# Performance work log

Measured on AMD Instinct MI355X. Metric: run time of the kernel, lower is better.

## Reference

```python
import jax, jax.numpy as jnp
import numpy as np

B, L, H, NH = 8, 384, 512, 8
DH = H // NH
MAX_SEQ_LEN = 384


def setup_inputs() -> dict:
    key = jax.random.key(0)
    ks = jax.random.split(key, 16)
    s = 0.02
    seq_len = jnp.concatenate([
        jnp.array([L], dtype=jnp.int32),
        jax.random.randint(ks[3], (B - 1,), L // 2, L + 1, dtype=jnp.int32),
    ])
    return {
        "key": jax.random.normal(ks[0], (B, L, H), jnp.float32),
        "query": jax.random.normal(ks[1], (B, L, H), jnp.float32),
        "value": jax.random.normal(ks[2], (B, L, H), jnp.float32),
        "seq_len": seq_len,
        "pe": jax.random.normal(ks[4], (2 * MAX_SEQ_LEN + 1, H), jnp.float32) * s,
        "Wk": jax.random.normal(ks[5], (H, H), jnp.float32) * s,
        "bk": jnp.zeros((H,), jnp.float32),
        "Wq": jax.random.normal(ks[6], (H, H), jnp.float32) * s,
        "bq": jnp.zeros((H,), jnp.float32),
        "Wv": jax.random.normal(ks[7], (H, H), jnp.float32) * s,
        "bv": jnp.zeros((H,), jnp.float32),
        "Wr": jax.random.normal(ks[8], (H, H), jnp.float32) * s,
        "br": jnp.zeros((H,), jnp.float32),
        "u_bias": jax.random.normal(ks[9], (NH, DH), jnp.float32) * s,
        "v_bias": jax.random.normal(ks[10], (NH, DH), jnp.float32) * s,
        "Wff": jax.random.normal(ks[11], (H, H), jnp.float32) * s,
        "bff": jnp.zeros((H,), jnp.float32),
    }


def reference(key, query, value, seq_len, pe, Wk, bk, Wq, bq, Wv, bv, Wr, br, u_bias, v_bias, Wff, bff):
    # relative distances: rel[i, j] = j - i, in [-(L-1), L-1]
    rel = jnp.arange(L)[None, :] - jnp.arange(L)[:, None]          # [L, L]
    rpe = pe[rel + MAX_SEQ_LEN]                                    # [L, L, H]

    k = (key @ Wk.T + bk).reshape(B, L, NH, DH)
    q = (query @ Wq.T + bq).reshape(B, L, NH, DH)
    v = (value @ Wv.T + bv).reshape(B, L, NH, DH)
    rpe = (rpe @ Wr.T + br).reshape(L, L, NH, DH)

    # Transformer-XL score terms
    A = jnp.einsum('bihd,bjhd->bhij', q, k)                        # content-content
    Bt = jnp.einsum('bihd,ijhd->bhij', q, rpe)                     # content-position
    C = jnp.einsum('hd,bjhd->bhj', u_bias, k)[:, :, None, :]       # global content bias
    Dt = jnp.einsum('hd,ijhd->hij', v_bias, rpe)[None]             # global position bias

    scores = (A + Bt + C + Dt) / jnp.sqrt(jnp.float32(DH))
    key_mask = jnp.arange(L)[None, :] < seq_len[:, None]           # [B, L]
    scores = jnp.where(key_mask[:, None, None, :], scores, -1e15)
    attn = jax.nn.softmax(scores, axis=-1)                         # [B, NH, L, L]

    out = jnp.einsum('bhij,bjhd->bihd', attn, v).reshape(B, L, H)
    return out @ Wff.T + bff
```

## Files before the change

### kernel.cpp

```cpp
#include <hip/hip_runtime.h>
#include <hip/hip_bf16.h>

#define B_  8
#define L_  384
#define H_  512
#define NH_ 8
#define DH_ 64
#define RRM 768

typedef short bf16x8 __attribute__((ext_vector_type(8)));
typedef float f32x4  __attribute__((ext_vector_type(4)));
#define MFMA_BF16 __builtin_amdgcn_mfma_f32_16x16x32_bf16

static __device__ __forceinline__ unsigned short f2bf(float f) {
    unsigned u = __builtin_bit_cast(unsigned, f);
    u += 0x7fffu + ((u >> 16) & 1u);
    return (unsigned short)(u >> 16);
}
static __device__ __forceinline__ float bf2f(unsigned short s) {
    unsigned u = ((unsigned)s) << 16;
    return __builtin_bit_cast(float, u);
}

typedef unsigned int u32;
static __device__ __forceinline__ void glds16(const void* g, void* l) {
    __builtin_amdgcn_global_load_lds(
        (const __attribute__((address_space(1))) u32*)g,
        (__attribute__((address_space(3))) u32*)l, 16, 0, 0);
}

struct CvtArgs {
    const float* src[9];
    unsigned short* dst[9];
    int nchunks[9];
};
__global__ __launch_bounds__(256) void cvt_kernel(CvtArgs a) {
    int chunk = blockIdx.x;
    int r = 0;
    while (r < 8 && chunk >= a.nchunks[r]) { chunk -= a.nchunks[r]; r++; }
    const float4 v = ((const float4*)a.src[r])[chunk * 256 + threadIdx.x];
    ushort4 o;
    o.x = f2bf(v.x); o.y = f2bf(v.y); o.z = f2bf(v.z); o.w = f2bf(v.w);
    ((ushort4*)a.dst[r])[chunk * 256 + threadIdx.x] = o;
}

template <bool IS_FF>
__global__ __launch_bounds__(256) void gemm_nt(
    const unsigned short* __restrict__ A0, const unsigned short* __restrict__ A1,
    const unsigned short* __restrict__ A2, const unsigned short* __restrict__ A3,
    const unsigned short* __restrict__ A4,
    const unsigned short* __restrict__ W0, const unsigned short* __restrict__ W1,
    const unsigned short* __restrict__ W2, const unsigned short* __restrict__ W3,
    const unsigned short* __restrict__ W4,
    const float* __restrict__ b0, const float* __restrict__ b1,
    const float* __restrict__ b2, const float* __restrict__ b3,
    const float* __restrict__ b4,
    const float* __restrict__ ub, const float* __restrict__ vbias,
    unsigned short* __restrict__ qu, unsigned short* __restrict__ qv,
    unsigned short* __restrict__ kb, unsigned short* __restrict__ vT,
    unsigned short* __restrict__ rp, float* __restrict__ ff) {

    const int z = IS_FF ? 4 : blockIdx.z;
    if (!IS_FF && z == 3 && blockIdx.y >= 12) return;
    const unsigned short* A = z == 0 ? A0 : z == 1 ? A1 : z == 2 ? A2 : z == 3 ? A3 : A4;
    const unsigned short* W = z == 0 ? W0 : z == 1 ? W1 : z == 2 ? W2 : z == 3 ? W3 : W4;
    const float* bias       = z == 0 ? b0 : z == 1 ? b1 : z == 2 ? b2 : z == 3 ? b3 : b4;

    __shared__ unsigned short AsF[2 * 64 * 64];
    __shared__ unsigned short BsF[2 * 64 * 64];

    const int tid = threadIdx.x;
    const int w = tid >> 6, lane = tid & 63;
    const int quad = lane >> 4, lm = lane & 15;
    const int wr = (w & 1) * 32, wc = (w >> 1) * 32;

    const int sr = lane >> 3, sj = lane & 7;
    const unsigned short* ga = A + (size_t)(blockIdx.y * 64 + w * 16 + sr) * 512 + (sj ^ sr) * 8;
    const unsigned short* gb = W + (size_t)(blockIdx.x * 64 + w * 16 + sr) * 512 + (sj ^ sr) * 8;

    auto stage = [&](int kc, int buf) {
        #pragma unroll
        for (int t = 0; t < 2; ++t) {
            int off = buf * 4096 + (w * 16 + t * 8) * 64;
            off = __builtin_amdgcn_readfirstlane(off);
            glds16(ga + kc * 64 + t * 8 * 512, &AsF[off]);
            glds16(gb + kc * 64 + t * 8 * 512, &BsF[off]);
        }
    };

    f32x4 acc[2][2] = {};
    stage(0, 0);
    for (int kc = 0; kc < 8; ++kc) {
        __syncthreads();
        const int buf = kc & 1;
        if (kc < 7) stage(kc + 1, buf ^ 1);
        const int base = buf * 4096;
        #pragma unroll
        for (int ks = 0; ks < 2; ++ks) {
            const int s = (((ks * 4 + quad) ^ (lm & 7))) * 8;
            bf16x8 a0 = *(const bf16x8*)&AsF[base + (wr + lm) * 64 + s];
            bf16x8 a1 = *(const bf16x8*)&AsF[base + (wr + 16 + lm) * 64 + s];
            bf16x8 w0 = *(const bf16x8*)&BsF[base + (wc + lm) * 64 + s];
            bf16x8 w1 = *(const bf16x8*)&BsF[base + (wc + 16 + lm) * 64 + s];
            acc[0][0] = MFMA_BF16(a0, w0, acc[0][0], 0, 0, 0);
            acc[0][1] = MFMA_BF16(a0, w1, acc[0][1], 0, 0, 0);
            acc[1][0] = MFMA_BF16(a1, w0, acc[1][0], 0, 0, 0);
            acc[1][1] = MFMA_BF16(a1, w1, acc[1][1], 0, 0, 0);
        }
    }

    #pragma unroll
    for (int si = 0; si < 2; ++si) {
        #pragma unroll
        for (int sj2 = 0; sj2 < 2; ++sj2) {
            #pragma unroll
            for (int reg = 0; reg < 4; ++reg) {
                const int r = blockIdx.y * 64 + wr + si * 16 + quad * 4 + reg;
                const int c = blockIdx.x * 64 + wc + sj2 * 16 + lm;
                const float val = acc[si][sj2][reg] + bias[c];
                if (IS_FF) {
                    ff[r * 512 + c] = val;
                } else if (z == 0) {
                    const int bb = r / L_, ii = r - bb * L_;
                    const int h = c >> 6, d = c & 63;
                    const int idx = ((bb * NH_ + h) * L_ + ii) * DH_ + d;
                    qu[idx] = f2bf((val + ub[c]) * 0.125f);
                    qv[idx] = f2bf((val + vbias[c]) * 0.125f);
                } else if (z == 1) {
                    const int bb = r / L_, ii = r - bb * L_;
                    const int h = c >> 6, d = c & 63;
                    kb[((bb * NH_ + h) * L_ + ii) * DH_ + d] = f2bf(val);
                } else if (z == 2) {
                    const int bb = r / L_, ii = r - bb * L_;
                    const int h = c >> 6, d = c & 63;
                    vT[((bb * NH_ + h) * DH_ + d) * L_ + ii] = f2bf(val);
                } else {
                    rp[r * 512 + c] = f2bf(val);
                }
            }
        }
    }
}

#define BTSTR 424
__global__ __launch_bounds__(256) void attn_fused(
    const unsigned short* __restrict__ qu, const unsigned short* __restrict__ qv,
    const unsigned short* __restrict__ kbf, const unsigned short* __restrict__ vT,
    const unsigned short* __restrict__ rp, const int* __restrict__ seq_len,
    unsigned short* __restrict__ Obf) {
    __shared__ __align__(16) unsigned short BtP[32 * BTSTR];
    __shared__ float mx_red[32][2];
    __shared__ float sm_red[32][2];
    const int lane = threadIdx.x & 63, wv = threadIdx.x >> 6;
    const int quad = lane >> 4, lm = lane & 15;
    const int bh = blockIdx.y, b = bh >> 3, h = bh & 7;
    const int i0 = blockIdx.x * 32;
    const int sl = seq_len[b];
    const int msub = wv & 1, nh = wv >> 1;
    const int m_lo = 353 - i0;
    const int i_fr = i0 + msub * 16 + lm;

    {
        const unsigned short* qvr = qv + (size_t)(bh * L_ + i_fr) * DH_;
        const bf16x8 av0 = *(const bf16x8*)(qvr + quad * 8);
        const bf16x8 av1 = *(const bf16x8*)(qvr + 32 + quad * 8);
        #pragma unroll
        for (int ns = 0; ns < 13; ++ns) {
            const int ntl = nh * 208 + ns * 16;
            if (ntl <= sl + 30) {
                const int n = ntl + lm;
                const unsigned short* rrow = rp + (size_t)(m_lo + n) * 512 + h * 64;
                f32x4 bacc = {};
                bacc = MFMA_BF16(av0, *(const bf16x8*)(rrow + quad * 8), bacc, 0, 0, 0);
                bacc = MFMA_BF16(av1, *(const bf16x8*)(rrow + 32 + quad * 8), bacc, 0, 0, 0);
                #pragma unroll
                for (int reg = 0; reg < 4; ++reg) {
                    const int il = msub * 16 + quad * 4 + reg;
                    BtP[il * BTSTR + n] = f2bf(bacc[reg]);
                }
            }
        }
    }
    const unsigned short* qur = qu + (size_t)(bh * L_ + i_fr) * DH_;
    const bf16x8 au0 = *(const bf16x8*)(qur + quad * 8);
    const bf16x8 au1 = *(const bf16x8*)(qur + 32 + quad * 8);
    __syncthreads();

    f32x4 sc[12];
    #pragma unroll
    for (int ns = 0; ns < 12; ++ns) {
        const int jt = nh * 192 + ns * 16;
        if (jt < sl) {
            const unsigned short* krow = kbf + (size_t)(bh * L_ + jt + lm) * DH_;
            f32x4 a = {};
            a = MFMA_BF16(au0, *(const bf16x8*)(krow + quad * 8), a, 0, 0, 0);
            a = MFMA_BF16(au1, *(const bf16x8*)(krow + 32 + quad * 8), a, 0, 0, 0);
            sc[ns] = a;
        } else {
            sc[ns] = f32x4{-1e30f, -1e30f, -1e30f, -1e30f};
        }
    }
    const int jbase = nh * 192 + lm;
    #pragma unroll
    for (int ns = 0; ns < 12; ++ns) {
        const int j = jbase + ns * 16;
        #pragma unroll
        for (int reg = 0; reg < 4; ++reg) {
            const int il = msub * 16 + quad * 4 + reg;
            float val = -1e30f;
            if (j < sl) val = sc[ns][reg] + bf2f(BtP[il * BTSTR + (j - il + 31)]);
            sc[ns][reg] = val;
        }
    }

    const int il0 = msub * 16 + quad * 4;
    float mx4[4], sm4[4], inv4[4];
    #pragma unroll
    for (int reg = 0; reg < 4; ++reg) {
        float m = sc[0][reg];
        #pragma unroll
        for (int ns = 1; ns < 12; ++ns) m = fmaxf(m, sc[ns][reg]);
        #pragma unroll
        for (int o = 1; o < 16; o <<= 1) m = fmaxf(m, __shfl_xor(m, o));
        mx4[reg] = m;
    }
    if (lm == 0) {
        #pragma unroll
        for (int reg = 0; reg < 4; ++reg) mx_red[il0 + reg][nh] = mx4[reg];
    }
    __syncthreads();
    #pragma unroll
    for (int reg = 0; reg < 4; ++reg)
        mx4[reg] = fmaxf(mx_red[il0 + reg][0], mx_red[il0 + reg][1]);
    #pragma unroll
    for (int reg = 0; reg < 4; ++reg) sm4[reg] = 0.f;
    #pragma unroll
    for (int ns = 0; ns < 12; ++ns) {
        #pragma unroll
        for (int reg = 0; reg < 4; ++reg) {
            const float e = __expf(sc[ns][reg] - mx4[reg]);
            sc[ns][reg] = e;
            sm4[reg] += e;
        }
    }
    #pragma unroll
    for (int reg = 0; reg < 4; ++reg) {
        float s = sm4[reg];
        #pragma unroll
        for (int o = 1; o < 16; o <<= 1) s += __shfl_xor(s, o);
        sm4[reg] = s;
    }
    if (lm == 0) {
        #pragma unroll
        for (int reg = 0; reg < 4; ++reg) sm_red[il0 + reg][nh] = sm4[reg];
    }
    __syncthreads();
    #pragma unroll
    for (int reg = 0; reg < 4; ++reg)
        inv4[reg] = 1.f / (sm_red[il0 + reg][0] + sm_red[il0 + reg][1]);

    #pragma unroll
    for (int ns = 0; ns < 12; ++ns) {
        const int j = jbase + ns * 16;
        #pragma unroll
        for (int reg = 0; reg < 4; ++reg)
            BtP[(il0 + reg) * BTSTR + j] = f2bf(sc[ns][reg] * inv4[reg]);
    }
    __syncthreads();

    {
        const int pr = msub * 16 + lm;
        const int nkc = (sl + 31) >> 5;
        f32x4 oacc[2] = {};
        for (int kc = 0; kc < nkc; ++kc) {
            const bf16x8 af = *(const bf16x8*)&BtP[pr * BTSTR + kc * 32 + quad * 8];
            #pragma unroll
            for (int t = 0; t < 2; ++t) {
                const int n = nh * 32 + t * 16 + lm;
                const unsigned short* vrow = vT + (size_t)(bh * DH_ + n) * L_ + kc * 32 + quad * 8;
                oacc[t] = MFMA_BF16(af, *(const bf16x8*)(vrow), oacc[t], 0, 0, 0);
            }
        }
        #pragma unroll
        for (int t = 0; t < 2; ++t) {
            #pragma unroll
            for (int reg = 0; reg < 4; ++reg) {
                const int i = i0 + msub * 16 + quad * 4 + reg;
                const int d = nh * 32 + t * 16 + lm;
                Obf[(size_t)(b * L_ + i) * H_ + h * DH_ + d] = f2bf(oacc[t][reg]);
            }
        }
    }
}

extern "C" void kernel_launch(void* const* d_in, const int* in_sizes, int n_in,
                              void* d_out, int out_size, void* d_ws, size_t ws_size,
                              hipStream_t stream) {
    const float* key    = (const float*)d_in[0];
    const float* query  = (const float*)d_in[1];
    const float* value  = (const float*)d_in[2];
    const int*   seqlen = (const int*)d_in[3];
    const float* pe     = (const float*)d_in[4];
    const float* Wk     = (const float*)d_in[5];
    const float* bk     = (const float*)d_in[6];
    const float* Wq     = (const float*)d_in[7];
    const float* bq     = (const float*)d_in[8];
    const float* Wv     = (const float*)d_in[9];
    const float* bv     = (const float*)d_in[10];
    const float* Wr     = (const float*)d_in[11];
    const float* br     = (const float*)d_in[12];
    const float* u_bias = (const float*)d_in[13];
    const float* v_bias = (const float*)d_in[14];
    const float* Wff    = (const float*)d_in[15];
    const float* bff    = (const float*)d_in[16];

    const size_t nTok = (size_t)B_ * L_ * H_;
    const size_t nPe  = (size_t)RRM * H_;
    const size_t nW   = (size_t)H_ * H_;
    unsigned short* p  = (unsigned short*)d_ws;
    unsigned short* qbf  = p; p += nTok;
    unsigned short* kin  = p; p += nTok;
    unsigned short* vin  = p; p += nTok;
    unsigned short* pebf = p; p += nPe;
    unsigned short* Wqb  = p; p += nW;
    unsigned short* Wkb  = p; p += nW;
    unsigned short* Wvb  = p; p += nW;
    unsigned short* Wrb  = p; p += nW;
    unsigned short* Wffb = p; p += nW;
    unsigned short* qu   = p; p += nTok;
    unsigned short* qv   = p; p += nTok;
    unsigned short* kb   = p; p += nTok;
    unsigned short* vT   = p; p += nTok;
    unsigned short* rp   = p; p += nPe + 512;
    unsigned short* Obf  = qbf;

    CvtArgs ca;
    ca.src[0] = query;  ca.dst[0] = qbf;  ca.nchunks[0] = 1536;
    ca.src[1] = key;    ca.dst[1] = kin;  ca.nchunks[1] = 1536;
    ca.src[2] = value;  ca.dst[2] = vin;  ca.nchunks[2] = 1536;
    ca.src[3] = pe;     ca.dst[3] = pebf; ca.nchunks[3] = 384;
    ca.src[4] = Wq;     ca.dst[4] = Wqb;  ca.nchunks[4] = 256;
    ca.src[5] = Wk;     ca.dst[5] = Wkb;  ca.nchunks[5] = 256;
    ca.src[6] = Wv;     ca.dst[6] = Wvb;  ca.nchunks[6] = 256;
    ca.src[7] = Wr;     ca.dst[7] = Wrb;  ca.nchunks[7] = 256;
    ca.src[8] = Wff;    ca.dst[8] = Wffb; ca.nchunks[8] = 256;
    cvt_kernel<<<6272, 256, 0, stream>>>(ca);

    gemm_nt<false><<<dim3(8, 48, 4), 256, 0, stream>>>(
         qbf, kin, vin, pebf, nullptr,
         Wqb, Wkb, Wvb, Wrb, nullptr,
         bq, bk, bv, br, nullptr,
         u_bias, v_bias,
         qu, qv, kb, vT, rp,
         nullptr);

    attn_fused<<<dim3(L_ / 32, B_ * NH_), 256, 0, stream>>>(
        qu, qv, kb, vT, rp, seqlen, Obf);

    gemm_nt<true><<<dim3(8, 48, 1), 256, 0, stream>>>(
         nullptr, nullptr, nullptr, nullptr, Obf,
         nullptr, nullptr, nullptr, nullptr, Wffb,
         nullptr, nullptr, nullptr, nullptr, bff,
         nullptr, nullptr,
         nullptr, nullptr, nullptr, nullptr, nullptr,
         (float*)d_out);
}
```

Baseline: 160.7 us.

## Fuse fp32-to-bf16 conversion into GEMM tile loads, drop separate convert kernel

Removes the standalone conversion kernel that turned inputs, positional embeddings and weights into bf16 in workspace. The GEMMs now load fp32 tiles into registers, convert them with packed bf16 conversion instructions, and write them swizzled into LDS, using register prefetch in place of direct global-to-LDS loads. This avoids a full extra read and write pass over all inputs and one kernel launch. In exchange each GEMM block reads fp32 (twice the bytes), weights are reconverted by every block that uses them, and the load pipeline now goes through registers.

```diff
diff --git a/kernel.cpp b/kernel.cpp
--- a/kernel.cpp
+++ b/kernel.cpp
@@ -1,5 +1,4 @@
 #include <hip/hip_runtime.h>
-#include <hip/hip_bf16.h>
 
 #define B_  8
 #define L_  384
@@ -10,6 +9,8 @@
 
 typedef short bf16x8 __attribute__((ext_vector_type(8)));
 typedef float f32x4  __attribute__((ext_vector_type(4)));
+typedef unsigned int u32;
+typedef u32 u32x4 __attribute__((ext_vector_type(4)));
 #define MFMA_BF16 __builtin_amdgcn_mfma_f32_16x16x32_bf16
 
 static __device__ __forceinline__ unsigned short f2bf(float f) {
@@ -21,37 +22,20 @@
     unsigned u = ((unsigned)s) << 16;
     return __builtin_bit_cast(float, u);
 }
-
-typedef unsigned int u32;
-static __device__ __forceinline__ void glds16(const void* g, void* l) {
-    __builtin_amdgcn_global_load_lds(
-        (const __attribute__((address_space(1))) u32*)g,
-        (__attribute__((address_space(3))) u32*)l, 16, 0, 0);
-}
-
-struct CvtArgs {
-    const float* src[9];
-    unsigned short* dst[9];
-    int nchunks[9];
-};
-__global__ __launch_bounds__(256) void cvt_kernel(CvtArgs a) {
-    int chunk = blockIdx.x;
-    int r = 0;
-    while (r < 8 && chunk >= a.nchunks[r]) { chunk -= a.nchunks[r]; r++; }
-    const float4 v = ((const float4*)a.src[r])[chunk * 256 + threadIdx.x];
-    ushort4 o;
-    o.x = f2bf(v.x); o.y = f2bf(v.y); o.z = f2bf(v.z); o.w = f2bf(v.w);
-    ((ushort4*)a.dst[r])[chunk * 256 + threadIdx.x] = o;
+static __device__ __forceinline__ u32 pk2(float lo, float hi) {
+    u32 r;
+    asm("v_cvt_pk_bf16_f32 %0, %1, %2" : "=v"(r) : "v"(lo), "v"(hi));
+    return r;
 }
 
 template <bool IS_FF>
 __global__ __launch_bounds__(256) void gemm_nt(
-    const unsigned short* __restrict__ A0, const unsigned short* __restrict__ A1,
-    const unsigned short* __restrict__ A2, const unsigned short* __restrict__ A3,
-    const unsigned short* __restrict__ A4,
-    const unsigned short* __restrict__ W0, const unsigned short* __restrict__ W1,
-    const unsigned short* __restrict__ W2, const unsigned short* __restrict__ W3,
-    const unsigned short* __restrict__ W4,
+    const float* __restrict__ A0, const float* __restrict__ A1,
+    const float* __restrict__ A2, const float* __restrict__ A3,
+    const unsigned short* __restrict__ Abf,
+    const float* __restrict__ W0, const float* __restrict__ W1,
+    const float* __restrict__ W2, const float* __restrict__ W3,
+    const float* __restrict__ W4,
     const float* __restrict__ b0, const float* __restrict__ b1,
     const float* __restrict__ b2, const float* __restrict__ b3,
     const float* __restrict__ b4,
@@ -62,12 +46,12 @@
 
     const int z = IS_FF ? 4 : blockIdx.z;
     if (!IS_FF && z == 3 && blockIdx.y >= 12) return;
-    const unsigned short* A = z == 0 ? A0 : z == 1 ? A1 : z == 2 ? A2 : z == 3 ? A3 : A4;
-    const unsigned short* W = z == 0 ? W0 : z == 1 ? W1 : z == 2 ? W2 : z == 3 ? W3 : W4;
-    const float* bias       = z == 0 ? b0 : z == 1 ? b1 : z == 2 ? b2 : z == 3 ? b3 : b4;
-
-    __shared__ unsigned short AsF[2 * 64 * 64];
-    __shared__ unsigned short BsF[2 * 64 * 64];
+    const float* Af   = z == 0 ? A0 : z == 1 ? A1 : z == 2 ? A2 : A3;
+    const float* W    = z == 0 ? W0 : z == 1 ? W1 : z == 2 ? W2 : z == 3 ? W3 : W4;
+    const float* bias = z == 0 ? b0 : z == 1 ? b1 : z == 2 ? b2 : z == 3 ? b3 : b4;
+
+    __shared__ __align__(16) unsigned short AsF[2 * 64 * 64];
+    __shared__ __align__(16) unsigned short BsF[2 * 64 * 64];
 
     const int tid = threadIdx.x;
     const int w = tid >> 6, lane = tid & 63;
@@ -75,25 +59,58 @@
     const int wr = (w & 1) * 32, wc = (w >> 1) * 32;
 
     const int sr = lane >> 3, sj = lane & 7;
-    const unsigned short* ga = A + (size_t)(blockIdx.y * 64 + w * 16 + sr) * 512 + (sj ^ sr) * 8;
-    const unsigned short* gb = W + (size_t)(blockIdx.x * 64 + w * 16 + sr) * 512 + (sj ^ sr) * 8;
-
-    auto stage = [&](int kc, int buf) {
+    const size_t aoff = (size_t)(blockIdx.y * 64 + w * 16 + sr) * 512 + sj * 8;
+    const size_t boff = (size_t)(blockIdx.x * 64 + w * 16 + sr) * 512 + sj * 8;
+
+    f32x4 la[2][2], lb[2][2];
+    bf16x8 lah[2];
+
+    auto LOAD = [&](int kc) {
         #pragma unroll
         for (int t = 0; t < 2; ++t) {
-            int off = buf * 4096 + (w * 16 + t * 8) * 64;
-            off = __builtin_amdgcn_readfirstlane(off);
-            glds16(ga + kc * 64 + t * 8 * 512, &AsF[off]);
-            glds16(gb + kc * 64 + t * 8 * 512, &BsF[off]);
+            if constexpr (IS_FF) {
+                lah[t] = *(const bf16x8*)(Abf + aoff + t * 8 * 512 + kc * 64);
+            } else {
+                const float* p = Af + aoff + t * 8 * 512 + kc * 64;
+                la[t][0] = *(const f32x4*)p;
+                la[t][1] = *(const f32x4*)(p + 4);
+            }
+            const float* q = W + boff + t * 8 * 512 + kc * 64;
+            lb[t][0] = *(const f32x4*)q;
+            lb[t][1] = *(const f32x4*)(q + 4);
         }
     };
+    auto WRITE = [&](int buf) {
+        #pragma unroll
+        for (int t = 0; t < 2; ++t) {
+            const int off = buf * 4096 + (w * 16 + t * 8 + sr) * 64 + (sj ^ sr) * 8;
+            if constexpr (IS_FF) {
+                *(bf16x8*)&AsF[off] = lah[t];
+            } else {
+                u32x4 pa;
+                pa[0] = pk2(la[t][0][0], la[t][0][1]);
+                pa[1] = pk2(la[t][0][2], la[t][0][3]);
+                pa[2] = pk2(la[t][1][0], la[t][1][1]);
+                pa[3] = pk2(la[t][1][2], la[t][1][3]);
+                *(u32x4*)&AsF[off] = pa;
+            }
+            u32x4 pb;
+            pb[0] = pk2(lb[t][0][0], lb[t][0][1]);
+            pb[1] = pk2(lb[t][0][2], lb[t][0][3]);
+            pb[2] = pk2(lb[t][1][0], lb[t][1][1]);
+            pb[3] = pk2(lb[t][1][2], lb[t][1][3]);
+            *(u32x4*)&BsF[off] = pb;
+        }
+    };
 
     f32x4 acc[2][2] = {};
-    stage(0, 0);
+    LOAD(0);
+    #pragma unroll 2
     for (int kc = 0; kc < 8; ++kc) {
+        const int buf = kc & 1;
+        WRITE(buf);
+        if (kc < 7) LOAD(kc + 1);
         __syncthreads();
-        const int buf = kc & 1;
-        if (kc < 7) stage(kc + 1, buf ^ 1);
         const int base = buf * 4096;
         #pragma unroll
         for (int ks = 0; ks < 2; ++ks) {
@@ -316,39 +333,17 @@
 
     const size_t nTok = (size_t)B_ * L_ * H_;
     const size_t nPe  = (size_t)RRM * H_;
-    const size_t nW   = (size_t)H_ * H_;
     unsigned short* p  = (unsigned short*)d_ws;
-    unsigned short* qbf  = p; p += nTok;
-    unsigned short* kin  = p; p += nTok;
-    unsigned short* vin  = p; p += nTok;
-    unsigned short* pebf = p; p += nPe;
-    unsigned short* Wqb  = p; p += nW;
-    unsigned short* Wkb  = p; p += nW;
-    unsigned short* Wvb  = p; p += nW;
-    unsigned short* Wrb  = p; p += nW;
-    unsigned short* Wffb = p; p += nW;
     unsigned short* qu   = p; p += nTok;
     unsigned short* qv   = p; p += nTok;
     unsigned short* kb   = p; p += nTok;
     unsigned short* vT   = p; p += nTok;
     unsigned short* rp   = p; p += nPe + 512;
-    unsigned short* Obf  = qbf;
-
-    CvtArgs ca;
-    ca.src[0] = query;  ca.dst[0] = qbf;  ca.nchunks[0] = 1536;
-    ca.src[1] = key;    ca.dst[1] = kin;  ca.nchunks[1] = 1536;
-    ca.src[2] = value;  ca.dst[2] = vin;  ca.nchunks[2] = 1536;
-    ca.src[3] = pe;     ca.dst[3] = pebf; ca.nchunks[3] = 384;
-    ca.src[4] = Wq;     ca.dst[4] = Wqb;  ca.nchunks[4] = 256;
-    ca.src[5] = Wk;     ca.dst[5] = Wkb;  ca.nchunks[5] = 256;
-    ca.src[6] = Wv;     ca.dst[6] = Wvb;  ca.nchunks[6] = 256;
-    ca.src[7] = Wr;     ca.dst[7] = Wrb;  ca.nchunks[7] = 256;
-    ca.src[8] = Wff;    ca.dst[8] = Wffb; ca.nchunks[8] = 256;
-    cvt_kernel<<<6272, 256, 0, stream>>>(ca);
+    unsigned short* Obf  = p; p += nTok;
 
     gemm_nt<false><<<dim3(8, 48, 4), 256, 0, stream>>>(
-         qbf, kin, vin, pebf, nullptr,
-         Wqb, Wkb, Wvb, Wrb, nullptr,
+         query, key, value, pe,  nullptr,
+         Wq, Wk, Wv, Wr, nullptr,
          bq, bk, bv, br, nullptr,
          u_bias, v_bias,
          qu, qv, kb, vT, rp,
@@ -358,8 +353,8 @@
         qu, qv, kb, vT, rp, seqlen, Obf);
 
     gemm_nt<true><<<dim3(8, 48, 1), 256, 0, stream>>>(
-         nullptr, nullptr, nullptr, nullptr, Obf,
-         nullptr, nullptr, nullptr, nullptr, Wffb,
+         nullptr, nullptr, nullptr, nullptr,  Obf,
+         nullptr, nullptr, nullptr, nullptr, Wff,
          nullptr, nullptr, nullptr, nullptr, bff,
          nullptr, nullptr,
          nullptr, nullptr, nullptr, nullptr, nullptr,
```

Result: no change. 158.5 us (-1.4%).
